# Kernel tuning notes

Measured on AMD Instinct MI355X. Metric: run time of the kernel, lower is better.

## Reference

```python
import jax, jax.numpy as jnp
import numpy as np

HEADS = 16
DIM_HEAD = 64
SCALE = DIM_HEAD ** -0.5


def setup_inputs() -> dict:
    key = jax.random.key(0)
    k1, k2, k3 = jax.random.split(key, 3)
    B, N, D = 4, 4096, 1024
    inner = HEADS * DIM_HEAD  # 1024
    x = jax.random.normal(k1, (B, N, D), dtype=jnp.float32)
    w_qkv = jax.random.normal(k2, (D, 3 * inner), dtype=jnp.float32) * (D ** -0.5)
    w_out = jax.random.normal(k3, (inner, D), dtype=jnp.float32) * (inner ** -0.5)
    b_out = jnp.zeros((D,), dtype=jnp.float32)
    return {"x": x, "w_qkv": w_qkv, "w_out": w_out, "b_out": b_out}


def reference(x, w_qkv, w_out, b_out):
    B, N, D = x.shape
    inner = HEADS * DIM_HEAD
    qkv = x @ w_qkv  # [B, N, 3*inner]
    q, k, v = jnp.split(qkv, 3, axis=-1)

    def to_heads(t):  # [B, N, inner] -> [B, H, N, Dh]
        return t.reshape(B, N, HEADS, DIM_HEAD).transpose(0, 2, 1, 3)

    q, k, v = to_heads(q), to_heads(k), to_heads(v)
    q = jax.nn.softmax(q * SCALE, axis=-1)   # softmax over feature dim d
    k = jax.nn.softmax(k, axis=-2)           # softmax over sequence dim n
    # context[d, e] = sum_n q[n, d] * k[n, e]
    context = jnp.einsum('bhnd,bhne->bhde', q, k)
    # out[n, e] = sum_d context[d, e] * v[n, d]
    out = jnp.einsum('bhde,bhnd->bhne', context, v)
    out = out.transpose(0, 2, 1, 3).reshape(B, N, inner)  # [B, N, inner]
    return out @ w_out + b_out
```

## Files before the change

kernel.cpp:

```cpp
#include <hip/hip_runtime.h>
#include <hip/hip_bf16.h>

#define SEQ    4096
#define SCALE  0.125f

typedef __attribute__((ext_vector_type(8))) short s8v;
typedef __attribute__((ext_vector_type(4))) float f4v;

__device__ __forceinline__ unsigned short f2bf(float f){
  unsigned int u = __builtin_bit_cast(unsigned int, f);
  u += 0x7FFFu + ((u >> 16) & 1u);
  return (unsigned short)(u >> 16);
}
__device__ __forceinline__ float bf2f(unsigned short s){
  unsigned int u = ((unsigned int)s) << 16;
  return __builtin_bit_cast(float, u);
}

typedef const __attribute__((address_space(1))) unsigned int gl_uint;
typedef __attribute__((address_space(3))) unsigned int lds_uint;

__device__ __forceinline__ void gload_lds16(const unsigned short* g, unsigned short* l){
  __builtin_amdgcn_global_load_lds((gl_uint*)g, (lds_uint*)l, 16, 0, 0);
}

__global__ __launch_bounds__(256, 4) void qkv_gemm(
    const unsigned short* __restrict__ A,
    const unsigned short* __restrict__ Bt,
    unsigned short* __restrict__ qt,
    unsigned short* __restrict__ kt,
    unsigned short* __restrict__ vb)
{
  __shared__ unsigned short sA[128*32];
  __shared__ unsigned short sB[128*32];
  const int K = 1024;
  const int tid  = threadIdx.x;
  const int wave = tid >> 6, lane = tid & 63;
  const int quad = lane >> 4, l16 = lane & 15;
  const int bm = blockIdx.y * 128, bn = blockIdx.x * 128;
  const int wm = (wave >> 1) * 64, wn = (wave & 1) * 64;

  f4v acc[4][4];
#pragma unroll
  for (int i = 0; i < 4; i++)
#pragma unroll
    for (int j = 0; j < 4; j++) acc[i][j] = (f4v){0.f,0.f,0.f,0.f};

  const unsigned short* ap = A  + (size_t)(bm + (tid >> 2)) * K + (tid & 3) * 8;
  const unsigned short* bp = Bt + (size_t)(bn + (tid >> 2)) * K + (tid & 3) * 8;
  unsigned short* sAw = sA + wave * 512;
  unsigned short* sBw = sB + wave * 512;

  for (int k0 = 0; k0 < K; k0 += 32){
    __syncthreads();
    gload_lds16(ap + k0,                    sAw);
    gload_lds16(ap + (size_t)64 * K + k0,   sAw + 2048);
    gload_lds16(bp + k0,                    sBw);
    gload_lds16(bp + (size_t)64 * K + k0,   sBw + 2048);
    __syncthreads();
    s8v af[4], bf[4];
#pragma unroll
    for (int mt = 0; mt < 4; mt++) af[mt] = *(const s8v*)&sA[(wm + mt*16 + l16)*32 + quad*8];
#pragma unroll
    for (int nt = 0; nt < 4; nt++) bf[nt] = *(const s8v*)&sB[(wn + nt*16 + l16)*32 + quad*8];
#pragma unroll
    for (int mt = 0; mt < 4; mt++)
#pragma unroll
      for (int nt = 0; nt < 4; nt++)
        acc[mt][nt] = __builtin_amdgcn_mfma_f32_16x16x32_bf16(af[mt], bf[nt], acc[mt][nt], 0, 0, 0);
  }

  const int colbase = bn + wn;
  const int sec = colbase >> 10;

  if (sec == 2){
#pragma unroll
    for (int nt = 0; nt < 4; nt++){
      int vc = colbase + nt*16 + l16 - 2048;
#pragma unroll
      for (int mt = 0; mt < 4; mt++){
        int row = bm + wm + mt*16 + quad*4;
#pragma unroll
        for (int r = 0; r < 4; r++)
          vb[(size_t)(row + r) * 1024 + vc] = f2bf(acc[mt][nt][r]);
      }
    }
    return;
  }

  if (sec == 0){
#pragma unroll
    for (int mt = 0; mt < 4; mt++){
#pragma unroll
      for (int r = 0; r < 4; r++){
        float m = fmaxf(fmaxf(acc[mt][0][r], acc[mt][1][r]),
                        fmaxf(acc[mt][2][r], acc[mt][3][r]));
        for (int off = 8; off; off >>= 1) m = fmaxf(m, __shfl_xor(m, off));
        m *= SCALE;
        float e0 = __expf(acc[mt][0][r] * SCALE - m);
        float e1 = __expf(acc[mt][1][r] * SCALE - m);
        float e2 = __expf(acc[mt][2][r] * SCALE - m);
        float e3 = __expf(acc[mt][3][r] * SCALE - m);
        float s = (e0 + e1) + (e2 + e3);
        for (int off = 8; off; off >>= 1) s += __shfl_xor(s, off);
        float inv = 1.f / s;
        acc[mt][0][r] = e0 * inv; acc[mt][1][r] = e1 * inv;
        acc[mt][2][r] = e2 * inv; acc[mt][3][r] = e3 * inv;
      }
    }
#pragma unroll
    for (int nt = 0; nt < 4; nt++){
      int col = colbase + nt*16 + l16;
      int h = (col >> 6) & 15;
      int de = col & 63;
#pragma unroll
      for (int mt = 0; mt < 4; mt++){
        int row = bm + wm + mt*16 + quad*4;
        int bb = row >> 12;
        int nl = row & 4095;
        ushort4 o;
        o.x = f2bf(acc[mt][nt][0]); o.y = f2bf(acc[mt][nt][1]);
        o.z = f2bf(acc[mt][nt][2]); o.w = f2bf(acc[mt][nt][3]);
        *(ushort4*)&qt[(((size_t)bb * 16 + h) * 64 + de) * SEQ + nl] = o;
      }
    }
  } else {
#pragma unroll
    for (int nt = 0; nt < 4; nt++){
      int col = colbase + nt*16 + l16;
      int h = (col >> 6) & 15;
      int de = col & 63;
#pragma unroll
      for (int mt = 0; mt < 4; mt++){
        int row = bm + wm + mt*16 + quad*4;
        int bb = row >> 12;
        int nl = row & 4095;
        ushort4 o;
        o.x = f2bf(__expf(acc[mt][nt][0])); o.y = f2bf(__expf(acc[mt][nt][1]));
        o.z = f2bf(__expf(acc[mt][nt][2])); o.w = f2bf(__expf(acc[mt][nt][3]));
        *(ushort4*)&kt[(((size_t)bb * 16 + h) * 64 + de) * SEQ + nl] = o;
      }
    }
  }
}

__global__ __launch_bounds__(256) void gemm_final(
    const unsigned short* __restrict__ A,
    const unsigned short* __restrict__ C2t,
    float* __restrict__ Cf,
    const float* __restrict__ bias)
{
  __shared__ unsigned short sA[128*32];
  __shared__ unsigned short sB[128*32];
  const int K = 1024;
  const int tid  = threadIdx.x;
  const int wave = tid >> 6, lane = tid & 63;
  const int quad = lane >> 4, l16 = lane & 15;
  const int bm = blockIdx.y * 128, bn = blockIdx.x * 128;
  const int b  = blockIdx.y >> 5;
  const unsigned short* Bt = C2t + (size_t)b * 1024 * 1024;
  const int wm = (wave >> 1) * 64, wn = (wave & 1) * 64;

  f4v acc[4][4];
#pragma unroll
  for (int i = 0; i < 4; i++)
#pragma unroll
    for (int j = 0; j < 4; j++) acc[i][j] = (f4v){0.f,0.f,0.f,0.f};

  const unsigned short* ap = A  + (size_t)(bm + (tid >> 2)) * K + (tid & 3) * 8;
  const unsigned short* bp = Bt + (size_t)(bn + (tid >> 2)) * K + (tid & 3) * 8;
  unsigned short* sAw = sA + wave * 512;
  unsigned short* sBw = sB + wave * 512;

  for (int k0 = 0; k0 < K; k0 += 32){
    __syncthreads();
    gload_lds16(ap + k0,                    sAw);
    gload_lds16(ap + (size_t)64 * K + k0,   sAw + 2048);
    gload_lds16(bp + k0,                    sBw);
    gload_lds16(bp + (size_t)64 * K + k0,   sBw + 2048);
    __syncthreads();
    s8v af[4], bf[4];
#pragma unroll
    for (int mt = 0; mt < 4; mt++) af[mt] = *(const s8v*)&sA[(wm + mt*16 + l16)*32 + quad*8];
#pragma unroll
    for (int nt = 0; nt < 4; nt++) bf[nt] = *(const s8v*)&sB[(wn + nt*16 + l16)*32 + quad*8];
#pragma unroll
    for (int mt = 0; mt < 4; mt++)
#pragma unroll
      for (int nt = 0; nt < 4; nt++)
        acc[mt][nt] = __builtin_amdgcn_mfma_f32_16x16x32_bf16(af[mt], bf[nt], acc[mt][nt], 0, 0, 0);
  }

#pragma unroll
  for (int nt = 0; nt < 4; nt++){
    int col = bn + wn + nt*16 + l16;
    float bv = bias[col];
#pragma unroll
    for (int mt = 0; mt < 4; mt++){
      int row = bm + wm + mt*16 + quad*4;
#pragma unroll
      for (int r = 0; r < 4; r++)
        Cf[(size_t)(row + r) * 1024 + col] = acc[mt][nt][r] + bv;
    }
  }
}

__global__ void cvt_f32_bf16(const float4* __restrict__ in, ushort4* __restrict__ outp){
  int i = blockIdx.x * 256 + threadIdx.x;
  float4 v = in[i];
  ushort4 o;
  o.x = f2bf(v.x); o.y = f2bf(v.y); o.z = f2bf(v.z); o.w = f2bf(v.w);
  outp[i] = o;
}

__global__ __launch_bounds__(256) void transpose_cvt(const float* __restrict__ in,
                                                     unsigned short* __restrict__ outp,
                                                     int R, int C){
  __shared__ float tile[64][65];
  int r0 = blockIdx.y * 64, c0 = blockIdx.x * 64;
  int t = threadIdx.x;
  for (int i = t; i < 4096; i += 256){ int r = i >> 6, c = i & 63;
    tile[r][c] = in[(size_t)(r0 + r) * C + c0 + c]; }
  __syncthreads();
  for (int i = t; i < 4096; i += 256){ int c = i >> 6, r = i & 63;
    outp[(size_t)(c0 + c) * R + r0 + r] = f2bf(tile[r][c]); }
}

__global__ __launch_bounds__(256) void ctx_partial(const unsigned short* __restrict__ qt,
                                                   const unsigned short* __restrict__ kt,
                                                   float* __restrict__ ctxp){
  __shared__ float red[4096];
  int bh = blockIdx.x >> 2, ch = blockIdx.x & 3;
  int t = threadIdx.x, wave = t >> 6, lane = t & 63, quad = lane >> 4, l16 = lane & 15;
  const unsigned short* qb = qt + (size_t)bh * 64 * SEQ;
  const unsigned short* kb = kt + (size_t)bh * 64 * SEQ;
  f4v acc[4][4];
#pragma unroll
  for (int i = 0; i < 4; i++)
#pragma unroll
    for (int j = 0; j < 4; j++) acc[i][j] = (f4v){0.f,0.f,0.f,0.f};
  int ns = ch * 1024 + wave * 256;
  for (int n0 = ns; n0 < ns + 256; n0 += 32){
    s8v af[4], bf[4];
#pragma unroll
    for (int mt = 0; mt < 4; mt++) af[mt] = *(const s8v*)&qb[(size_t)(mt*16 + l16) * SEQ + n0 + quad*8];
#pragma unroll
    for (int nt = 0; nt < 4; nt++) bf[nt] = *(const s8v*)&kb[(size_t)(nt*16 + l16) * SEQ + n0 + quad*8];
#pragma unroll
    for (int mt = 0; mt < 4; mt++)
#pragma unroll
      for (int nt = 0; nt < 4; nt++)
        acc[mt][nt] = __builtin_amdgcn_mfma_f32_16x16x32_bf16(af[mt], bf[nt], acc[mt][nt], 0, 0, 0);
  }
  for (int i = t; i < 4096; i += 256) red[i] = 0.f;
  __syncthreads();
  for (int w = 0; w < 4; w++){
    if (wave == w){
#pragma unroll
      for (int mt = 0; mt < 4; mt++)
#pragma unroll
        for (int nt = 0; nt < 4; nt++)
#pragma unroll
          for (int r = 0; r < 4; r++)
            red[(mt*16 + quad*4 + r) * 64 + nt*16 + l16] += acc[mt][nt][r];
    }
    __syncthreads();
  }
  float* cp = ctxp + (size_t)blockIdx.x * 4096;
  for (int i = t; i < 4096; i += 256) cp[i] = red[i];
}

__global__ __launch_bounds__(256) void ctx2_kernel(const float* __restrict__ ctxp,
                                                   const float* __restrict__ w_out,
                                                   unsigned short* __restrict__ ctx2t){
  __shared__ float ctxs[4096];
  __shared__ float inv_s[64];
  int bh = blockIdx.x >> 4, fc = blockIdx.x & 15;
  int b = bh >> 4, h = bh & 15;
  int t = threadIdx.x;
  int fl = t & 63, dg = t >> 6;
  int f = fc * 64 + fl;
  for (int i = t; i < 4096; i += 256){
    const float* p = ctxp + (size_t)bh * 4 * 4096 + i;
    ctxs[i] = (p[0] + p[4096]) + (p[8192] + p[12288]);
  }
  __syncthreads();
  if (t < 64){
    float s = 0.f;
#pragma unroll
    for (int d = 0; d < 64; d++) s += ctxs[d * 64 + t];
    inv_s[t] = 1.f / s;
  }
  __syncthreads();
  float acc[16];
#pragma unroll
  for (int i = 0; i < 16; i++) acc[i] = 0.f;
  for (int e = 0; e < 64; e++){
    float w = w_out[(size_t)(h * 64 + e) * 1024 + f] * inv_s[e];
#pragma unroll
    for (int dd = 0; dd < 16; dd++)
      acc[dd] += ctxs[(dg * 16 + dd) * 64 + e] * w;
  }
  unsigned short* op = ctx2t + ((size_t)b * 1024 + f) * 1024 + h * 64 + dg * 16;
#pragma unroll
  for (int g = 0; g < 4; g++){
    ushort4 o;
    o.x = f2bf(acc[g*4+0]); o.y = f2bf(acc[g*4+1]);
    o.z = f2bf(acc[g*4+2]); o.w = f2bf(acc[g*4+3]);
    *(ushort4*)&op[g*4] = o;
  }
}

extern "C" void kernel_launch(void* const* d_in, const int* in_sizes, int n_in,
                              void* d_out, int out_size, void* d_ws, size_t ws_size,
                              hipStream_t stream) {
  const float* x     = (const float*)d_in[0];
  const float* w_qkv = (const float*)d_in[1];
  const float* w_out = (const float*)d_in[2];
  const float* b_out = (const float*)d_in[3];
  float* out = (float*)d_out;

  const int M = 4 * SEQ;

  unsigned short* xb = (unsigned short*)d_out;

  char* wp = (char*)d_ws;
  size_t off = 0;
  auto nxt = [&](size_t bytes) -> char* {
    char* p = wp + off;
    off += (bytes + 255) & ~(size_t)255;
    return p;
  };
  unsigned short* wqkvT = (unsigned short*)nxt((size_t)3072 * 1024 * 2);
  unsigned short* qt    = (unsigned short*)nxt((size_t)64 * 64 * SEQ * 2);
  unsigned short* kt    = (unsigned short*)nxt((size_t)64 * 64 * SEQ * 2);
  unsigned short* vb    = (unsigned short*)nxt((size_t)M * 1024 * 2);
  float*          ctxp  = (float*)wqkvT;
  unsigned short* ctx2t = qt;

  cvt_f32_bf16<<<(M * 1024) / 4 / 256, 256, 0, stream>>>((const float4*)x, (ushort4*)xb);
  transpose_cvt<<<dim3(3072 / 64, 1024 / 64), 256, 0, stream>>>(w_qkv, wqkvT, 1024, 3072);

  qkv_gemm<<<dim3(3072 / 128, M / 128), 256, 0, stream>>>(xb, wqkvT, qt, kt, vb);

  ctx_partial<<<64 * 4, 256, 0, stream>>>(qt, kt, ctxp);

  ctx2_kernel<<<64 * 16, 256, 0, stream>>>(ctxp, w_out, ctx2t);

  gemm_final<<<dim3(1024 / 128, M / 128), 256, 0, stream>>>(vb, ctx2t, out, b_out);
}
```

Measured before the change: 379.1 us.

## Rewrite both GEMMs with 256x256 tiles and a 4-stage LDS pipeline

Both GEMM kernels move onto a shared mainloop that uses 256x256 block tiles with 8 waves, a 4-deep ring of LDS buffers filled by direct global-to-LDS loads, XOR-swizzled LDS layout, split-phase MFMA scheduling with explicit waitcnt, barriers and setprio, plus a grouped block-index swizzle for L2 locality. The aim is to hide global-load latency behind MFMA work, avoid LDS bank conflicts and raise arithmetic intensity per tile compared with the old single-buffered 128x128 loop. In exchange it needs 128 KB of LDS per block and a large accumulator register footprint. The hand-tuned vmcnt counts are fragile and correctness depends on them, and fewer blocks are launched, which may leave some CUs idle.

```diff
diff --git a/kernel.cpp b/kernel.cpp
--- a/kernel.cpp
+++ b/kernel.cpp
@@ -12,10 +12,6 @@
   u += 0x7FFFu + ((u >> 16) & 1u);
   return (unsigned short)(u >> 16);
 }
-__device__ __forceinline__ float bf2f(unsigned short s){
-  unsigned int u = ((unsigned int)s) << 16;
-  return __builtin_bit_cast(float, u);
-}
 
 typedef const __attribute__((address_space(1))) unsigned int gl_uint;
 typedef __attribute__((address_space(3))) unsigned int lds_uint;
@@ -24,65 +20,142 @@
   __builtin_amdgcn_global_load_lds((gl_uint*)g, (lds_uint*)l, 16, 0, 0);
 }
 
-__global__ __launch_bounds__(256, 4) void qkv_gemm(
+#define MM(a,b,c) __builtin_amdgcn_mfma_f32_16x16x32_bf16(a,b,c,0,0,0)
+#define BAR() __builtin_amdgcn_s_barrier()
+#define LGKM0() do{ asm volatile("s_waitcnt lgkmcnt(0)" ::: "memory"); \
+                    __builtin_amdgcn_sched_barrier(0); }while(0)
+#define VMW(n) asm volatile("s_waitcnt vmcnt(" #n ")" ::: "memory")
+
+__device__ __forceinline__ void mainloop_256(
+    const unsigned short* __restrict__ Ag,
+    const unsigned short* __restrict__ Bg,
+    int bm, int bn, f4v (&acc)[8][4])
+{
+  __shared__ __align__(16) unsigned short lds[65536];
+  const int tid  = threadIdx.x;
+  const int wave = tid >> 6, lane = tid & 63;
+  const int quad = lane >> 4, l16 = lane & 15;
+  const int wmi  = wave >> 2, wni = wave & 3;
+
+  const int schunk = (((tid & 3) ^ ((tid >> 4) & 3)) * 8);
+  const unsigned short* aS = Ag + (size_t)(bm + (tid >> 2)) * 1024 + schunk;
+  const unsigned short* bS = Bg + (size_t)(bn + (tid >> 2)) * 1024 + schunk;
+  unsigned short* ldsw = lds + wave * 512;
+
+  int aoff[8], boff[4];
+#pragma unroll
+  for (int mf = 0; mf < 8; mf++){
+    int r = wmi * 128 + mf * 16 + l16;
+    aoff[mf] = r * 32 + ((quad ^ ((r >> 2) & 3)) * 8);
+  }
+#pragma unroll
+  for (int nf = 0; nf < 4; nf++){
+    int c = wni * 64 + nf * 16 + l16;
+    boff[nf] = 8192 + c * 32 + ((quad ^ ((c >> 2) & 3)) * 8);
+  }
+
+#define STG_A(t_) do{ unsigned short* d_ = ldsw + ((t_) & 3) * 16384; \
+    const unsigned short* s_ = aS + (t_) * 32; \
+    gload_lds16(s_, d_); gload_lds16(s_ + 128 * 1024, d_ + 4096); }while(0)
+#define STG_B(t_) do{ unsigned short* d_ = ldsw + ((t_) & 3) * 16384 + 8192; \
+    const unsigned short* s_ = bS + (t_) * 32; \
+    gload_lds16(s_, d_); gload_lds16(s_ + 128 * 1024, d_ + 4096); }while(0)
+
+  STG_A(0); STG_B(0); STG_A(1); STG_B(1); STG_A(2); STG_B(2);
+  VMW(8); BAR();
+
+  s8v a0, a1, a2, a3, b0, b1, b2, b3;
+
+#define PH_A(t_, STG) do{ \
+    const unsigned short* base_ = lds + ((t_) & 3) * 16384; \
+    b0 = *(const s8v*)(base_ + boff[0]); b1 = *(const s8v*)(base_ + boff[1]); \
+    b2 = *(const s8v*)(base_ + boff[2]); b3 = *(const s8v*)(base_ + boff[3]); \
+    a0 = *(const s8v*)(base_ + aoff[0]); a1 = *(const s8v*)(base_ + aoff[1]); \
+    a2 = *(const s8v*)(base_ + aoff[2]); a3 = *(const s8v*)(base_ + aoff[3]); \
+    if (STG) STG_A((t_) + 3); \
+    BAR(); LGKM0(); \
+    __builtin_amdgcn_s_setprio(1); \
+    acc[0][0]=MM(a0,b0,acc[0][0]); acc[0][1]=MM(a0,b1,acc[0][1]); \
+    acc[0][2]=MM(a0,b2,acc[0][2]); acc[0][3]=MM(a0,b3,acc[0][3]); \
+    acc[1][0]=MM(a1,b0,acc[1][0]); acc[1][1]=MM(a1,b1,acc[1][1]); \
+    acc[1][2]=MM(a1,b2,acc[1][2]); acc[1][3]=MM(a1,b3,acc[1][3]); \
+    acc[2][0]=MM(a2,b0,acc[2][0]); acc[2][1]=MM(a2,b1,acc[2][1]); \
+    acc[2][2]=MM(a2,b2,acc[2][2]); acc[2][3]=MM(a2,b3,acc[2][3]); \
+    acc[3][0]=MM(a3,b0,acc[3][0]); acc[3][1]=MM(a3,b1,acc[3][1]); \
+    acc[3][2]=MM(a3,b2,acc[3][2]); acc[3][3]=MM(a3,b3,acc[3][3]); \
+    __builtin_amdgcn_s_setprio(0); \
+    BAR(); }while(0)
+
+#define PH_B(t_, STG, VN) do{ \
+    const unsigned short* base_ = lds + ((t_) & 3) * 16384; \
+    a0 = *(const s8v*)(base_ + aoff[4]); a1 = *(const s8v*)(base_ + aoff[5]); \
+    a2 = *(const s8v*)(base_ + aoff[6]); a3 = *(const s8v*)(base_ + aoff[7]); \
+    if (STG) STG_B((t_) + 3); \
+    VMW(VN); \
+    BAR(); LGKM0(); \
+    __builtin_amdgcn_s_setprio(1); \
+    acc[4][0]=MM(a0,b0,acc[4][0]); acc[4][1]=MM(a0,b1,acc[4][1]); \
+    acc[4][2]=MM(a0,b2,acc[4][2]); acc[4][3]=MM(a0,b3,acc[4][3]); \
+    acc[5][0]=MM(a1,b0,acc[5][0]); acc[5][1]=MM(a1,b1,acc[5][1]); \
+    acc[5][2]=MM(a1,b2,acc[5][2]); acc[5][3]=MM(a1,b3,acc[5][3]); \
+    acc[6][0]=MM(a2,b0,acc[6][0]); acc[6][1]=MM(a2,b1,acc[6][1]); \
+    acc[6][2]=MM(a2,b2,acc[6][2]); acc[6][3]=MM(a2,b3,acc[6][3]); \
+    acc[7][0]=MM(a3,b0,acc[7][0]); acc[7][1]=MM(a3,b1,acc[7][1]); \
+    acc[7][2]=MM(a3,b2,acc[7][2]); acc[7][3]=MM(a3,b3,acc[7][3]); \
+    __builtin_amdgcn_s_setprio(0); \
+    BAR(); }while(0)
+
+  for (int t = 0; t < 29; ++t){
+    PH_A(t, 1);
+    PH_B(t, 1, 8);
+  }
+  PH_A(29, 0); PH_B(29, 0, 4);
+  PH_A(30, 0); PH_B(30, 0, 0);
+  PH_A(31, 0); PH_B(31, 0, 0);
+
+#undef PH_A
+#undef PH_B
+#undef STG_A
+#undef STG_B
+}
+
+__global__ __launch_bounds__(512, 2) void qkv_gemm(
     const unsigned short* __restrict__ A,
     const unsigned short* __restrict__ Bt,
     unsigned short* __restrict__ qt,
     unsigned short* __restrict__ kt,
     unsigned short* __restrict__ vb)
 {
-  __shared__ unsigned short sA[128*32];
-  __shared__ unsigned short sB[128*32];
-  const int K = 1024;
-  const int tid  = threadIdx.x;
+  const int id  = blockIdx.x;
+  const int swz = (id & 7) * 96 + (id >> 3);
+  const int bm  = (swz / 12) * 256, bn = (swz % 12) * 256;
+
+  f4v acc[8][4];
+#pragma unroll
+  for (int i = 0; i < 8; i++)
+#pragma unroll
+    for (int j = 0; j < 4; j++) acc[i][j] = (f4v){0.f,0.f,0.f,0.f};
+
+  mainloop_256(A, Bt, bm, bn, acc);
+
+  const int tid = threadIdx.x;
   const int wave = tid >> 6, lane = tid & 63;
   const int quad = lane >> 4, l16 = lane & 15;
-  const int bm = blockIdx.y * 128, bn = blockIdx.x * 128;
-  const int wm = (wave >> 1) * 64, wn = (wave & 1) * 64;
-
-  f4v acc[4][4];
-#pragma unroll
-  for (int i = 0; i < 4; i++)
-#pragma unroll
-    for (int j = 0; j < 4; j++) acc[i][j] = (f4v){0.f,0.f,0.f,0.f};
-
-  const unsigned short* ap = A  + (size_t)(bm + (tid >> 2)) * K + (tid & 3) * 8;
-  const unsigned short* bp = Bt + (size_t)(bn + (tid >> 2)) * K + (tid & 3) * 8;
-  unsigned short* sAw = sA + wave * 512;
-  unsigned short* sBw = sB + wave * 512;
-
-  for (int k0 = 0; k0 < K; k0 += 32){
-    __syncthreads();
-    gload_lds16(ap + k0,                    sAw);
-    gload_lds16(ap + (size_t)64 * K + k0,   sAw + 2048);
-    gload_lds16(bp + k0,                    sBw);
-    gload_lds16(bp + (size_t)64 * K + k0,   sBw + 2048);
-    __syncthreads();
-    s8v af[4], bf[4];
-#pragma unroll
-    for (int mt = 0; mt < 4; mt++) af[mt] = *(const s8v*)&sA[(wm + mt*16 + l16)*32 + quad*8];
-#pragma unroll
-    for (int nt = 0; nt < 4; nt++) bf[nt] = *(const s8v*)&sB[(wn + nt*16 + l16)*32 + quad*8];
-#pragma unroll
-    for (int mt = 0; mt < 4; mt++)
-#pragma unroll
-      for (int nt = 0; nt < 4; nt++)
-        acc[mt][nt] = __builtin_amdgcn_mfma_f32_16x16x32_bf16(af[mt], bf[nt], acc[mt][nt], 0, 0, 0);
-  }
-
-  const int colbase = bn + wn;
+  const int wmi = wave >> 2, wni = wave & 3;
+  const int colbase = bn + wni * 64;
+  const int rowbase = bm + wmi * 128;
   const int sec = colbase >> 10;
 
   if (sec == 2){
 #pragma unroll
-    for (int nt = 0; nt < 4; nt++){
-      int vc = colbase + nt*16 + l16 - 2048;
-#pragma unroll
-      for (int mt = 0; mt < 4; mt++){
-        int row = bm + wm + mt*16 + quad*4;
+    for (int nf = 0; nf < 4; nf++){
+      int vc = colbase + nf * 16 + l16 - 2048;
+#pragma unroll
+      for (int mf = 0; mf < 8; mf++){
+        int row = rowbase + mf * 16 + quad * 4;
 #pragma unroll
         for (int r = 0; r < 4; r++)
-          vb[(size_t)(row + r) * 1024 + vc] = f2bf(acc[mt][nt][r]);
+          vb[(size_t)(row + r) * 1024 + vc] = f2bf(acc[mf][nf][r]);
       }
     }
     return;
@@ -90,117 +163,90 @@
 
   if (sec == 0){
 #pragma unroll
-    for (int mt = 0; mt < 4; mt++){
+    for (int mf = 0; mf < 8; mf++){
 #pragma unroll
       for (int r = 0; r < 4; r++){
-        float m = fmaxf(fmaxf(acc[mt][0][r], acc[mt][1][r]),
-                        fmaxf(acc[mt][2][r], acc[mt][3][r]));
+        float m = fmaxf(fmaxf(acc[mf][0][r], acc[mf][1][r]),
+                        fmaxf(acc[mf][2][r], acc[mf][3][r]));
         for (int off = 8; off; off >>= 1) m = fmaxf(m, __shfl_xor(m, off));
         m *= SCALE;
-        float e0 = __expf(acc[mt][0][r] * SCALE - m);
-        float e1 = __expf(acc[mt][1][r] * SCALE - m);
-        float e2 = __expf(acc[mt][2][r] * SCALE - m);
-        float e3 = __expf(acc[mt][3][r] * SCALE - m);
+        float e0 = __expf(acc[mf][0][r] * SCALE - m);
+        float e1 = __expf(acc[mf][1][r] * SCALE - m);
+        float e2 = __expf(acc[mf][2][r] * SCALE - m);
+        float e3 = __expf(acc[mf][3][r] * SCALE - m);
         float s = (e0 + e1) + (e2 + e3);
         for (int off = 8; off; off >>= 1) s += __shfl_xor(s, off);
         float inv = 1.f / s;
-        acc[mt][0][r] = e0 * inv; acc[mt][1][r] = e1 * inv;
-        acc[mt][2][r] = e2 * inv; acc[mt][3][r] = e3 * inv;
+        acc[mf][0][r] = e0 * inv; acc[mf][1][r] = e1 * inv;
+        acc[mf][2][r] = e2 * inv; acc[mf][3][r] = e3 * inv;
       }
     }
 #pragma unroll
-    for (int nt = 0; nt < 4; nt++){
-      int col = colbase + nt*16 + l16;
-      int h = (col >> 6) & 15;
-      int de = col & 63;
-#pragma unroll
-      for (int mt = 0; mt < 4; mt++){
-        int row = bm + wm + mt*16 + quad*4;
-        int bb = row >> 12;
-        int nl = row & 4095;
+    for (int nf = 0; nf < 4; nf++){
+      int col = colbase + nf * 16 + l16;
+      int h = (col >> 6) & 15, de = col & 63;
+#pragma unroll
+      for (int mf = 0; mf < 8; mf++){
+        int row = rowbase + mf * 16 + quad * 4;
+        int bb = row >> 12, nl = row & 4095;
         ushort4 o;
-        o.x = f2bf(acc[mt][nt][0]); o.y = f2bf(acc[mt][nt][1]);
-        o.z = f2bf(acc[mt][nt][2]); o.w = f2bf(acc[mt][nt][3]);
+        o.x = f2bf(acc[mf][nf][0]); o.y = f2bf(acc[mf][nf][1]);
+        o.z = f2bf(acc[mf][nf][2]); o.w = f2bf(acc[mf][nf][3]);
         *(ushort4*)&qt[(((size_t)bb * 16 + h) * 64 + de) * SEQ + nl] = o;
       }
     }
   } else {
 #pragma unroll
-    for (int nt = 0; nt < 4; nt++){
-      int col = colbase + nt*16 + l16;
-      int h = (col >> 6) & 15;
-      int de = col & 63;
-#pragma unroll
-      for (int mt = 0; mt < 4; mt++){
-        int row = bm + wm + mt*16 + quad*4;
-        int bb = row >> 12;
-        int nl = row & 4095;
+    for (int nf = 0; nf < 4; nf++){
+      int col = colbase + nf * 16 + l16;
+      int h = (col >> 6) & 15, de = col & 63;
+#pragma unroll
+      for (int mf = 0; mf < 8; mf++){
+        int row = rowbase + mf * 16 + quad * 4;
+        int bb = row >> 12, nl = row & 4095;
         ushort4 o;
-        o.x = f2bf(__expf(acc[mt][nt][0])); o.y = f2bf(__expf(acc[mt][nt][1]));
-        o.z = f2bf(__expf(acc[mt][nt][2])); o.w = f2bf(__expf(acc[mt][nt][3]));
+        o.x = f2bf(__expf(acc[mf][nf][0])); o.y = f2bf(__expf(acc[mf][nf][1]));
+        o.z = f2bf(__expf(acc[mf][nf][2])); o.w = f2bf(__expf(acc[mf][nf][3]));
         *(ushort4*)&kt[(((size_t)bb * 16 + h) * 64 + de) * SEQ + nl] = o;
       }
     }
   }
 }
 
-__global__ __launch_bounds__(256) void gemm_final(
+__global__ __launch_bounds__(512, 2) void gemm_final(
     const unsigned short* __restrict__ A,
     const unsigned short* __restrict__ C2t,
     float* __restrict__ Cf,
     const float* __restrict__ bias)
 {
-  __shared__ unsigned short sA[128*32];
-  __shared__ unsigned short sB[128*32];
-  const int K = 1024;
-  const int tid  = threadIdx.x;
+  const int id  = blockIdx.x;
+  const int swz = (id & 7) * 32 + (id >> 3);
+  const int bm  = (swz >> 2) * 256, bn = (swz & 3) * 256;
+  const unsigned short* Bt = C2t + (size_t)(bm >> 12) * 1024 * 1024;
+
+  f4v acc[8][4];
+#pragma unroll
+  for (int i = 0; i < 8; i++)
+#pragma unroll
+    for (int j = 0; j < 4; j++) acc[i][j] = (f4v){0.f,0.f,0.f,0.f};
+
+  mainloop_256(A, Bt, bm, bn, acc);
+
+  const int tid = threadIdx.x;
   const int wave = tid >> 6, lane = tid & 63;
   const int quad = lane >> 4, l16 = lane & 15;
-  const int bm = blockIdx.y * 128, bn = blockIdx.x * 128;
-  const int b  = blockIdx.y >> 5;
-  const unsigned short* Bt = C2t + (size_t)b * 1024 * 1024;
-  const int wm = (wave >> 1) * 64, wn = (wave & 1) * 64;
-
-  f4v acc[4][4];
-#pragma unroll
-  for (int i = 0; i < 4; i++)
-#pragma unroll
-    for (int j = 0; j < 4; j++) acc[i][j] = (f4v){0.f,0.f,0.f,0.f};
-
-  const unsigned short* ap = A  + (size_t)(bm + (tid >> 2)) * K + (tid & 3) * 8;
-  const unsigned short* bp = Bt + (size_t)(bn + (tid >> 2)) * K + (tid & 3) * 8;
-  unsigned short* sAw = sA + wave * 512;
-  unsigned short* sBw = sB + wave * 512;
-
-  for (int k0 = 0; k0 < K; k0 += 32){
-    __syncthreads();
-    gload_lds16(ap + k0,                    sAw);
-    gload_lds16(ap + (size_t)64 * K + k0,   sAw + 2048);
-    gload_lds16(bp + k0,                    sBw);
-    gload_lds16(bp + (size_t)64 * K + k0,   sBw + 2048);
-    __syncthreads();
-    s8v af[4], bf[4];
-#pragma unroll
-    for (int mt = 0; mt < 4; mt++) af[mt] = *(const s8v*)&sA[(wm + mt*16 + l16)*32 + quad*8];
-#pragma unroll
-    for (int nt = 0; nt < 4; nt++) bf[nt] = *(const s8v*)&sB[(wn + nt*16 + l16)*32 + quad*8];
-#pragma unroll
-    for (int mt = 0; mt < 4; mt++)
-#pragma unroll
-      for (int nt = 0; nt < 4; nt++)
-        acc[mt][nt] = __builtin_amdgcn_mfma_f32_16x16x32_bf16(af[mt], bf[nt], acc[mt][nt], 0, 0, 0);
-  }
-
-#pragma unroll
-  for (int nt = 0; nt < 4; nt++){
-    int col = bn + wn + nt*16 + l16;
+  const int wmi = wave >> 2, wni = wave & 3;
+
+#pragma unroll
+  for (int nf = 0; nf < 4; nf++){
+    int col = bn + wni * 64 + nf * 16 + l16;
     float bv = bias[col];
 #pragma unroll
-    for (int mt = 0; mt < 4; mt++){
-      int row = bm + wm + mt*16 + quad*4;
+    for (int mf = 0; mf < 8; mf++){
+      int row = bm + wmi * 128 + mf * 16 + quad * 4;
 #pragma unroll
       for (int r = 0; r < 4; r++)
-        Cf[(size_t)(row + r) * 1024 + col] = acc[mt][nt][r] + bv;
+        Cf[(size_t)(row + r) * 1024 + col] = acc[mf][nf][r] + bv;
     }
   }
 }
@@ -341,11 +387,11 @@
   cvt_f32_bf16<<<(M * 1024) / 4 / 256, 256, 0, stream>>>((const float4*)x, (ushort4*)xb);
   transpose_cvt<<<dim3(3072 / 64, 1024 / 64), 256, 0, stream>>>(w_qkv, wqkvT, 1024, 3072);
 
-  qkv_gemm<<<dim3(3072 / 128, M / 128), 256, 0, stream>>>(xb, wqkvT, qt, kt, vb);
+  qkv_gemm<<<768, 512, 0, stream>>>(xb, wqkvT, qt, kt, vb);
 
   ctx_partial<<<64 * 4, 256, 0, stream>>>(qt, kt, ctxp);
 
   ctx2_kernel<<<64 * 16, 256, 0, stream>>>(ctxp, w_out, ctx2t);
 
-  gemm_final<<<dim3(1024 / 128, M / 128), 256, 0, stream>>>(vb, ctx2t, out, b_out);
-}
+  gemm_final<<<256, 512, 0, stream>>>(vb, ctx2t, out, b_out);
+}
```

Result: faster. 347.1 us (-8.4%).
